# Kernel tuning notes

Measured on AMD Instinct MI355X. Metric: run time of the kernel, lower is better.

Reference implementation:

```python
import math
import jax, jax.numpy as jnp
import numpy as np

N, E, H, D, NNZ = 32768, 512, 8, 64, 524288


def setup_inputs() -> dict:
    key = jax.random.key(0)
    ks = jax.random.split(key, 12)
    x = jax.random.normal(ks[0], (N, E), dtype=jnp.float32)
    row_index = jnp.sort(jax.random.randint(ks[1], (NNZ,), 0, N))
    col_index = jax.random.randint(ks[2], (NNZ,), 0, N)
    to_col_index = jax.random.randint(ks[3], (N,), 0, N)
    att_bias = jax.random.normal(ks[4], (H, NNZ), dtype=jnp.float32)
    # positive interatomic distances in ~[0.5, 5.5)
    dist = jax.random.uniform(ks[5], (NNZ,), dtype=jnp.float32) * 5.0 + 0.5
    pos = jax.random.normal(ks[6], (N, 3), dtype=jnp.float32)
    col_pos = jax.random.normal(ks[7], (N, 3), dtype=jnp.float32)
    s = 1.0 / math.sqrt(E)
    q_w = jax.random.normal(ks[8], (E, E), dtype=jnp.float32) * s
    q_b = jax.random.normal(ks[9], (E,), dtype=jnp.float32) * 0.02
    k_w = jax.random.normal(ks[10], (E, E), dtype=jnp.float32) * s
    k_b = jax.random.normal(ks[11], (E,), dtype=jnp.float32) * 0.02
    return {"x": x, "row_index": row_index, "col_index": col_index,
            "to_col_index": to_col_index, "att_bias": att_bias, "dist": dist,
            "pos": pos, "col_pos": col_pos,
            "q_w": q_w, "q_b": q_b, "k_w": k_w, "k_b": k_b}


def reference(x, row_index, col_index, to_col_index, att_bias, dist, pos, col_pos,
              q_w, q_b, k_w, k_b):
    n = x.shape[0]
    h = att_bias.shape[0]
    d = x.shape[1] // h
    # per-head projections: [N, H, D]
    q = (x @ q_w.T + q_b).reshape(n, h, d) * (1.0 / math.sqrt(d))
    k = (x @ k_w.T + k_b).reshape(n, h, d)[to_col_index]  # [Nk, H, D]
    # sparse (COO) masked q @ k^T plus additive bias -> per-edge logits [nnz, H]
    logits = jnp.einsum('ehd,ehd->eh', q[row_index], k[col_index]) + att_bias.T
    # sparse softmax over each query row (per head)
    m = jax.ops.segment_max(logits, row_index, num_segments=n)       # [N, H]
    p = jnp.exp(logits - m[row_index])
    z = jax.ops.segment_sum(p, row_index, num_segments=n)            # [N, H]
    att = p / z[row_index]                                           # [nnz, H]
    # distance-weighted attention (dist==0 -> contribution 0, as x/inf in torch)
    inv_d = jnp.where(dist == 0, 0.0, 1.0 / dist)
    att = att * inv_d[:, None]
    # sparse bmm against col_pos values and against ones
    cp = col_pos[col_index]                                          # [nnz, 3]
    dst_vec = jax.ops.segment_sum(att[:, :, None] * cp[:, None, :],
                                  row_index, num_segments=n)         # [N, H, 3]
    avg_inv_dist = jax.ops.segment_sum(att, row_index, num_segments=n)  # [N, H]
    src_vec = avg_inv_dist[..., None] * pos[:, None, :]              # [N, H, 3]
    v = dst_vec - src_vec
    norm = jnp.sqrt(jnp.sum(v * v, axis=-1, keepdims=True))
    feat3 = v / jnp.maximum(norm, 1e-12)                             # F.normalize
    feat = jnp.concatenate([feat3, avg_inv_dist[..., None]], axis=-1)  # [N, H, 4]
    return feat.reshape(n, h * 4)
```

## Files before the change

### kernel.cpp

```cpp
#include <hip/hip_runtime.h>
#include <math.h>
#include <stdint.h>

#define N_NODES 32768
#define E_DIM   512
#define H_HEADS 8
#define D_HEAD  64
#define NNZ_E   524288

typedef __attribute__((ext_vector_type(4))) float f32x4;
typedef __attribute__((ext_vector_type(8))) _Float16 f16x8;

__device__ __forceinline__ void async16(const void* g, void* l) {
  __builtin_amdgcn_global_load_lds(
      (const __attribute__((address_space(1))) void*)g,
      (__attribute__((address_space(3))) void*)l, 16, 0, 0);
}

__device__ __forceinline__ float dot8(const f16x8 a, const f16x8 b, float acc) {
#if __has_builtin(__builtin_amdgcn_fdot2)
  acc = __builtin_amdgcn_fdot2(__builtin_shufflevector(a, a, 0, 1),
                               __builtin_shufflevector(b, b, 0, 1), acc, false);
  acc = __builtin_amdgcn_fdot2(__builtin_shufflevector(a, a, 2, 3),
                               __builtin_shufflevector(b, b, 2, 3), acc, false);
  acc = __builtin_amdgcn_fdot2(__builtin_shufflevector(a, a, 4, 5),
                               __builtin_shufflevector(b, b, 4, 5), acc, false);
  acc = __builtin_amdgcn_fdot2(__builtin_shufflevector(a, a, 6, 7),
                               __builtin_shufflevector(b, b, 6, 7), acc, false);
#else
#pragma unroll
  for (int i = 0; i < 8; ++i) acc = fmaf((float)a[i], (float)b[i], acc);
#endif
  return acc;
}

__global__ __launch_bounds__(256) void prep_small(
    const float* __restrict__ x,
    const float* __restrict__ q_w, const float* __restrict__ k_w,
    _Float16* __restrict__ wq_h, _Float16* __restrict__ wk_h,
    _Float16* __restrict__ xs) {
  const int b = blockIdx.x;
  const float* src;
  _Float16* dst;
  int t;
  if (b < 128)      { src = q_w; dst = wq_h; t = b * 256 + threadIdx.x; }
  else if (b < 256) { src = k_w; dst = wk_h; t = (b - 128) * 256 + threadIdx.x; }
  else              { src = x;   dst = xs;   t = (b - 256) * 256 + threadIdx.x; }
  const int r = t >> 6;
  const int c8 = (t & 63) << 3;
  const float4 v0 = *(const float4*)(src + (size_t)r * 512 + c8);
  const float4 v1 = *(const float4*)(src + (size_t)r * 512 + c8 + 4);
  f16x8 o;
  o[0] = (_Float16)v0.x; o[1] = (_Float16)v0.y;
  o[2] = (_Float16)v0.z; o[3] = (_Float16)v0.w;
  o[4] = (_Float16)v1.x; o[5] = (_Float16)v1.y;
  o[6] = (_Float16)v1.z; o[7] = (_Float16)v1.w;
  *(f16x8*)(dst + (size_t)r * 512 + c8) = o;
}

__global__ __launch_bounds__(256) void gemm_mfma(
    const _Float16* __restrict__ xs,
    const _Float16* __restrict__ wqh,
    const _Float16* __restrict__ wkh,
    const float* __restrict__ q_b, const float* __restrict__ k_b,
    _Float16* __restrict__ qh, _Float16* __restrict__ kh,
    const int* __restrict__ row_index, const int* __restrict__ col_index,
    const int* __restrict__ to_col,
    int* __restrict__ row_start, int* __restrict__ ge) {
  __shared__ _Float16 Ah[128 * 32];
  __shared__ _Float16 Bh[128 * 32];
  const int b = blockIdx.x;

  if (b >= 2048) {
    const int e = (b - 2048) * 256 + threadIdx.x;
    if (e < NNZ_E) {
      ge[e] = to_col[col_index[e]];
      const int r0 = row_index[e];
      const int r1 = (e + 1 < NNZ_E) ? row_index[e + 1] : N_NODES;
      if (e == 0)
        for (int r = 0; r <= r0; ++r) row_start[r] = 0;
      for (int r = r0 + 1; r <= r1; ++r) row_start[r] = e + 1;
    }
    return;
  }

  const int tid = threadIdx.x;
  const int w = tid >> 6;
  const int l = tid & 63;

  const int j = b >> 3;
  const int mb = (b & 7) * 32 + (j >> 3);
  const int c = j & 7;
  const bool is_q = ((c & 1) == 0);
  const int bm = mb * 128;
  const int bn = (c >> 1) * 128;

  const _Float16* __restrict__ wmat = is_q ? wqh : wkh;
  const float* __restrict__ bias = is_q ? q_b : k_b;
  _Float16* __restrict__ outp = is_q ? qh : kh;
  const float oscale = is_q ? 0.125f : 1.0f;

  const int wm = (w & 1) * 64;
  const int wn = (w >> 1) * 64;

  f32x4 acc[4][4];
#pragma unroll
  for (int i = 0; i < 4; ++i)
#pragma unroll
    for (int jj = 0; jj < 4; ++jj) acc[i][jj] = (f32x4){0.f, 0.f, 0.f, 0.f};

  const int sr0 = w * 16 + (l >> 2);
  const int sr1 = sr0 + 64;
  const int sc = (((l & 3) ^ ((l >> 3) & 3)) << 3);
  const int fr = l & 15;
  const int fcs = ((((l >> 4) ^ ((fr >> 1) & 3)) & 3) << 3);

  const _Float16* __restrict__ wa = wmat + (size_t)bn * 512;
  const _Float16* __restrict__ xa = xs + (size_t)bm * 512;

  for (int k0 = 0; k0 < 512; k0 += 32) {
    async16(xa + (size_t)sr0 * 512 + k0 + sc, Ah + w * 512);
    async16(xa + (size_t)sr1 * 512 + k0 + sc, Ah + (w + 4) * 512);
    async16(wa + (size_t)sr0 * 512 + k0 + sc, Bh + w * 512);
    async16(wa + (size_t)sr1 * 512 + k0 + sc, Bh + (w + 4) * 512);
    __syncthreads();

    f16x8 av[4], bv[4];
#pragma unroll
    for (int i = 0; i < 4; ++i)
      av[i] = *(const f16x8*)(Ah + (wm + i * 16 + fr) * 32 + fcs);
#pragma unroll
    for (int i = 0; i < 4; ++i)
      bv[i] = *(const f16x8*)(Bh + (wn + i * 16 + fr) * 32 + fcs);
#pragma unroll
    for (int i = 0; i < 4; ++i)
#pragma unroll
      for (int jj = 0; jj < 4; ++jj)
        acc[i][jj] = __builtin_amdgcn_mfma_f32_16x16x32_f16(
            av[i], bv[jj], acc[i][jj], 0, 0, 0);
    __syncthreads();
  }

  const int cn = l & 15;
  const int cm4 = (l >> 4) * 4;
  float bvals[4];
#pragma unroll
  for (int jj = 0; jj < 4; ++jj) bvals[jj] = bias[bn + wn + jj * 16 + cn];
#pragma unroll
  for (int i = 0; i < 4; ++i) {
#pragma unroll
    for (int r = 0; r < 4; ++r) {
      const int m = bm + wm + i * 16 + cm4 + r;
      _Float16* op = outp + (size_t)m * 512 + bn + wn + cn;
#pragma unroll
      for (int jj = 0; jj < 4; ++jj) {
        op[jj * 16] = (_Float16)((acc[i][jj][r] + bvals[jj]) * oscale);
      }
    }
  }
}

__global__ __launch_bounds__(256) void row_fused(
    const _Float16* __restrict__ qh, const _Float16* __restrict__ kh,
    const int* __restrict__ row_start, const int* __restrict__ ge,
    const float* __restrict__ att_bias, const int* __restrict__ col_index,
    const float* __restrict__ dist, const float* __restrict__ pos,
    const float* __restrict__ col_pos, float* __restrict__ out) {
  const int r = blockIdx.x * 4 + (threadIdx.x >> 6);
  const int lane = threadIdx.x & 63;
  const int h = lane >> 3;
  const int start = row_start[r];
  const int end = row_start[r + 1];

  const f16x8 qv = *(const f16x8*)(qh + (size_t)r * E_DIM + lane * 8);
  const float* __restrict__ biasp = att_bias + (size_t)h * NNZ_E;

  float m = -INFINITY, l = 0.f, accw = 0.f, a0 = 0.f, a1 = 0.f, a2 = 0.f;

  auto edge_logit = [&](const f16x8 kv) -> float {
    float s = dot8(qv, kv, 0.f);
    s += __shfl_xor(s, 1);
    s += __shfl_xor(s, 2);
    s += __shfl_xor(s, 4);
    return s;
  };
  auto upd = [&](float logit, float dd, float c0, float c1, float c2) {
    const float w = (dd == 0.f) ? 0.f : __builtin_amdgcn_rcpf(dd);
    const float nm = fmaxf(m, logit);
    const float sc = __expf(m - nm);
    const float p = __expf(logit - nm);
    m = nm;
    l = fmaf(l, sc, p);
    const float pw = p * w;
    accw = fmaf(accw, sc, pw);
    a0 = fmaf(a0, sc, pw * c0);
    a1 = fmaf(a1, sc, pw * c1);
    a2 = fmaf(a2, sc, pw * c2);
  };

  int e = start;
  for (; e + 4 <= end; e += 4) {
    int g[4], cc[4];
    float dd[4], bb[4], cp[4][3];
    f16x8 kv[4];
#pragma unroll
    for (int i = 0; i < 4; ++i) g[i] = ge[e + i];
#pragma unroll
    for (int i = 0; i < 4; ++i)
      kv[i] = *(const f16x8*)(kh + (size_t)g[i] * E_DIM + lane * 8);
#pragma unroll
    for (int i = 0; i < 4; ++i) {
      cc[i] = col_index[e + i];
      dd[i] = dist[e + i];
      bb[i] = biasp[e + i];
    }
#pragma unroll
    for (int i = 0; i < 4; ++i) {
      cp[i][0] = col_pos[cc[i] * 3 + 0];
      cp[i][1] = col_pos[cc[i] * 3 + 1];
      cp[i][2] = col_pos[cc[i] * 3 + 2];
    }
    float s[4];
#pragma unroll
    for (int i = 0; i < 4; ++i) s[i] = edge_logit(kv[i]) + bb[i];
#pragma unroll
    for (int i = 0; i < 4; ++i) upd(s[i], dd[i], cp[i][0], cp[i][1], cp[i][2]);
  }
  for (; e < end; ++e) {
    const int g0 = ge[e];
    const f16x8 kv0 = *(const f16x8*)(kh + (size_t)g0 * E_DIM + lane * 8);
    const int c0 = col_index[e];
    const float dd0 = dist[e];
    const float bb0 = biasp[e];
    const float cp00 = col_pos[c0 * 3 + 0];
    const float cp01 = col_pos[c0 * 3 + 1];
    const float cp02 = col_pos[c0 * 3 + 2];
    const float s0 = edge_logit(kv0) + bb0;
    upd(s0, dd0, cp00, cp01, cp02);
  }

  if ((lane & 7) == 0) {
    const float invz = (l > 0.f) ? 1.f / l : 0.f;
    const float avg = accw * invz;
    const float v0 = a0 * invz - avg * pos[r * 3 + 0];
    const float v1 = a1 * invz - avg * pos[r * 3 + 1];
    const float v2 = a2 * invz - avg * pos[r * 3 + 2];
    const float nrm = sqrtf(v0 * v0 + v1 * v1 + v2 * v2);
    const float invn = 1.f / fmaxf(nrm, 1e-12f);
    float4 o;
    o.x = v0 * invn; o.y = v1 * invn; o.z = v2 * invn; o.w = avg;
    *(float4*)(out + (size_t)r * (H_HEADS * 4) + h * 4) = o;
  }
}

extern "C" void kernel_launch(void* const* d_in, const int* in_sizes, int n_in,
                              void* d_out, int out_size, void* d_ws,
                              size_t ws_size, hipStream_t stream) {
  const float* x        = (const float*)d_in[0];
  const int* row_index  = (const int*)d_in[1];
  const int* col_index  = (const int*)d_in[2];
  const int* to_col     = (const int*)d_in[3];
  const float* att_bias = (const float*)d_in[4];
  const float* dist     = (const float*)d_in[5];
  const float* pos      = (const float*)d_in[6];
  const float* col_pos  = (const float*)d_in[7];
  const float* q_w      = (const float*)d_in[8];
  const float* q_b      = (const float*)d_in[9];
  const float* k_w      = (const float*)d_in[10];
  const float* k_b      = (const float*)d_in[11];
  float* out = (float*)d_out;

  _Float16* qh = (_Float16*)d_ws;
  _Float16* kh = qh + (size_t)N_NODES * 512;
  _Float16* xs = kh + (size_t)N_NODES * 512;
  _Float16* wq_h = xs + (size_t)N_NODES * 512;
  _Float16* wk_h = wq_h + 512 * 512;
  int* row_start = (int*)(wk_h + 512 * 512);
  int* ge = row_start + (N_NODES + 1);

  prep_small<<<8448, 256, 0, stream>>>(x, q_w, k_w, wq_h, wk_h, xs);

  gemm_mfma<<<4096, 256, 0, stream>>>(xs, wq_h, wk_h, q_b, k_b, qh, kh,
                                      row_index, col_index, to_col,
                                      row_start, ge);

  row_fused<<<N_NODES / 4, 256, 0, stream>>>(qh, kh, row_start, ge, att_bias,
                                             col_index, dist, pos, col_pos,
                                             out);
}
```

Baseline: 268.3 us.

## Move index prep into conversion kernel and double-buffer key gathers in row kernel

```diff
diff --git a/kernel.cpp b/kernel.cpp
--- a/kernel.cpp
+++ b/kernel.cpp
@@ -37,42 +37,31 @@
 __global__ __launch_bounds__(256) void prep_small(
     const float* __restrict__ x,
     const float* __restrict__ q_w, const float* __restrict__ k_w,
-    _Float16* __restrict__ wq_h, _Float16* __restrict__ wk_h,
-    _Float16* __restrict__ xs) {
-  const int b = blockIdx.x;
-  const float* src;
-  _Float16* dst;
-  int t;
-  if (b < 128)      { src = q_w; dst = wq_h; t = b * 256 + threadIdx.x; }
-  else if (b < 256) { src = k_w; dst = wk_h; t = (b - 128) * 256 + threadIdx.x; }
-  else              { src = x;   dst = xs;   t = (b - 256) * 256 + threadIdx.x; }
-  const int r = t >> 6;
-  const int c8 = (t & 63) << 3;
-  const float4 v0 = *(const float4*)(src + (size_t)r * 512 + c8);
-  const float4 v1 = *(const float4*)(src + (size_t)r * 512 + c8 + 4);
-  f16x8 o;
-  o[0] = (_Float16)v0.x; o[1] = (_Float16)v0.y;
-  o[2] = (_Float16)v0.z; o[3] = (_Float16)v0.w;
-  o[4] = (_Float16)v1.x; o[5] = (_Float16)v1.y;
-  o[6] = (_Float16)v1.z; o[7] = (_Float16)v1.w;
-  *(f16x8*)(dst + (size_t)r * 512 + c8) = o;
-}
-
-__global__ __launch_bounds__(256) void gemm_mfma(
-    const _Float16* __restrict__ xs,
-    const _Float16* __restrict__ wqh,
-    const _Float16* __restrict__ wkh,
-    const float* __restrict__ q_b, const float* __restrict__ k_b,
-    _Float16* __restrict__ qh, _Float16* __restrict__ kh,
     const int* __restrict__ row_index, const int* __restrict__ col_index,
     const int* __restrict__ to_col,
+    _Float16* __restrict__ wq_h, _Float16* __restrict__ wk_h,
+    _Float16* __restrict__ xs,
     int* __restrict__ row_start, int* __restrict__ ge) {
-  __shared__ _Float16 Ah[128 * 32];
-  __shared__ _Float16 Bh[128 * 32];
   const int b = blockIdx.x;
-
-  if (b >= 2048) {
-    const int e = (b - 2048) * 256 + threadIdx.x;
+  if (b < 8448) {
+    const float* src;
+    _Float16* dst;
+    int t;
+    if (b < 128)      { src = q_w; dst = wq_h; t = b * 256 + threadIdx.x; }
+    else if (b < 256) { src = k_w; dst = wk_h; t = (b - 128) * 256 + threadIdx.x; }
+    else              { src = x;   dst = xs;   t = (b - 256) * 256 + threadIdx.x; }
+    const int r = t >> 6;
+    const int c8 = (t & 63) << 3;
+    const float4 v0 = *(const float4*)(src + (size_t)r * 512 + c8);
+    const float4 v1 = *(const float4*)(src + (size_t)r * 512 + c8 + 4);
+    f16x8 o;
+    o[0] = (_Float16)v0.x; o[1] = (_Float16)v0.y;
+    o[2] = (_Float16)v0.z; o[3] = (_Float16)v0.w;
+    o[4] = (_Float16)v1.x; o[5] = (_Float16)v1.y;
+    o[6] = (_Float16)v1.z; o[7] = (_Float16)v1.w;
+    *(f16x8*)(dst + (size_t)r * 512 + c8) = o;
+  } else {
+    const int e = (b - 8448) * 256 + threadIdx.x;
     if (e < NNZ_E) {
       ge[e] = to_col[col_index[e]];
       const int r0 = row_index[e];
@@ -81,13 +70,22 @@
         for (int r = 0; r <= r0; ++r) row_start[r] = 0;
       for (int r = r0 + 1; r <= r1; ++r) row_start[r] = e + 1;
     }
-    return;
-  }
-
+  }
+}
+
+__global__ __launch_bounds__(256) void gemm_mfma(
+    const _Float16* __restrict__ xs,
+    const _Float16* __restrict__ wqh,
+    const _Float16* __restrict__ wkh,
+    const float* __restrict__ q_b, const float* __restrict__ k_b,
+    _Float16* __restrict__ qh, _Float16* __restrict__ kh) {
+  __shared__ _Float16 Ah[128 * 32];
+  __shared__ _Float16 Bh[128 * 32];
   const int tid = threadIdx.x;
   const int w = tid >> 6;
   const int l = tid & 63;
 
+  const int b = blockIdx.x;
   const int j = b >> 3;
   const int mb = (b & 7) * 32 + (j >> 3);
   const int c = j & 7;
@@ -198,33 +196,48 @@
     a2 = fmaf(a2, sc, pw * c2);
   };
 
+  auto loadg = [&](int e0, f16x8* kv) {
+#pragma unroll
+    for (int i = 0; i < 4; ++i) {
+      const int g = ge[e0 + i];
+      kv[i] = *(const f16x8*)(kh + (size_t)g * E_DIM + lane * 8);
+    }
+  };
+  auto proc4 = [&](int e0, const f16x8* kv) {
+    float dd[4], bb[4];
+    int cc[4];
+#pragma unroll
+    for (int i = 0; i < 4; ++i) {
+      cc[i] = col_index[e0 + i];
+      dd[i] = dist[e0 + i];
+      bb[i] = biasp[e0 + i];
+    }
+    float s[4];
+#pragma unroll
+    for (int i = 0; i < 4; ++i) s[i] = edge_logit(kv[i]) + bb[i];
+#pragma unroll
+    for (int i = 0; i < 4; ++i) {
+      const float c0 = col_pos[cc[i] * 3 + 0];
+      const float c1 = col_pos[cc[i] * 3 + 1];
+      const float c2 = col_pos[cc[i] * 3 + 2];
+      upd(s[i], dd[i], c0, c1, c2);
+    }
+  };
+
+  f16x8 kA[4], kB[4];
   int e = start;
-  for (; e + 4 <= end; e += 4) {
-    int g[4], cc[4];
-    float dd[4], bb[4], cp[4][3];
-    f16x8 kv[4];
-#pragma unroll
-    for (int i = 0; i < 4; ++i) g[i] = ge[e + i];
-#pragma unroll
-    for (int i = 0; i < 4; ++i)
-      kv[i] = *(const f16x8*)(kh + (size_t)g[i] * E_DIM + lane * 8);
-#pragma unroll
-    for (int i = 0; i < 4; ++i) {
-      cc[i] = col_index[e + i];
-      dd[i] = dist[e + i];
-      bb[i] = biasp[e + i];
-    }
-#pragma unroll
-    for (int i = 0; i < 4; ++i) {
-      cp[i][0] = col_pos[cc[i] * 3 + 0];
-      cp[i][1] = col_pos[cc[i] * 3 + 1];
-      cp[i][2] = col_pos[cc[i] * 3 + 2];
-    }
-    float s[4];
-#pragma unroll
-    for (int i = 0; i < 4; ++i) s[i] = edge_logit(kv[i]) + bb[i];
-#pragma unroll
-    for (int i = 0; i < 4; ++i) upd(s[i], dd[i], cp[i][0], cp[i][1], cp[i][2]);
+  const int n4 = (end - start) >> 2;
+  int gi = 0;
+  if (n4 > 0) loadg(e, kA);
+  for (; gi + 2 <= n4; gi += 2, e += 8) {
+    loadg(e + 4, kB);
+    proc4(e, kA);
+    if (gi + 2 < n4) loadg(e + 8, kA);
+    proc4(e + 4, kB);
+  }
+  if (gi < n4) {
+    proc4(e, kA);
+    e += 4;
   }
   for (; e < end; ++e) {
     const int g0 = ge[e];
@@ -278,11 +291,10 @@
   int* row_start = (int*)(wk_h + 512 * 512);
   int* ge = row_start + (N_NODES + 1);
 
-  prep_small<<<8448, 256, 0, stream>>>(x, q_w, k_w, wq_h, wk_h, xs);
-
-  gemm_mfma<<<4096, 256, 0, stream>>>(xs, wq_h, wk_h, q_b, k_b, qh, kh,
-                                      row_index, col_index, to_col,
-                                      row_start, ge);
+  prep_small<<<8448 + NNZ_E / 256, 256, 0, stream>>>(
+      x, q_w, k_w, row_index, col_index, to_col, wq_h, wk_h, xs, row_start, ge);
+
+  gemm_mfma<<<2048, 256, 0, stream>>>(xs, wq_h, wk_h, q_b, k_b, qh, kh);
 
   row_fused<<<N_NODES / 4, 256, 0, stream>>>(qh, kh, row_start, ge, att_bias,
                                              col_index, dist, pos, col_pos,
```

Measured after the change: 261.1 us. -2.7%, faster.
